# Performance work log

Measured on AMD Instinct MI355X. Metric: run time of the kernel, lower is better.

Reference implementation:

```python
import jax, jax.numpy as jnp
import numpy as np

INPUT_DIM = 4096
BOTTLENECK = 32768
A = 2
K = 0.05
# eval-mode sparsity count: max(1, int(bottleneck * a * k))
K_COUNT = max(1, int(BOTTLENECK * A * K))  # 3276


def setup_inputs() -> dict:
    key = jax.random.key(0)
    kx, kw = jax.random.split(key)
    x = jax.random.normal(kx, (4096, INPUT_DIM), dtype=jnp.float32)
    # encoder weight [bottleneck, input_dim], like nn.Linear(input_dim, bottleneck)
    W = jax.random.normal(kw, (BOTTLENECK, INPUT_DIM), dtype=jnp.float32) * (1.0 / np.sqrt(INPUT_DIM))
    b_enc = jnp.zeros((BOTTLENECK,), dtype=jnp.float32)
    b_dec = jnp.zeros((INPUT_DIM,), dtype=jnp.float32)
    return {"x": x, "W": W, "b_enc": b_enc, "b_dec": b_dec, "epoch": 0}


def reference(x, W, b_enc, b_dec, epoch):
    # encode: z1 = x @ W^T + b_enc  -> [B, bottleneck]
    z1 = jnp.einsum("bi,hi->bh", x, W) + b_enc
    # eval-mode k-winner-take-all mask over dim 1
    _, topk_idx = jax.lax.top_k(z1, K_COUNT)  # [B, K_COUNT]
    rows = jnp.arange(z1.shape[0])[:, None]
    mask = jnp.zeros_like(z1).at[rows, topk_idx].set(1.0)
    a1 = z1 * mask
    # tied-weight decode: z2 = a1 @ W + b_dec -> [B, input_dim]
    z2 = jnp.einsum("bh,hi->bi", a1, W) + b_dec
    return z2
```

## Files before the change

kernel.cpp:

```cpp
#include <hip/hip_runtime.h>
#include <hip/hip_bf16.h>
#include <stdint.h>


#define DIM      4096
#define BATCH    4096
#define NROWS_W  32768
#define KCNT     3276
#define DELTA    0.0025f
#define ROWCAP   256
#define HCAP     64
#define CANDCAP  3584

typedef _Float16 f16x8 __attribute__((ext_vector_type(8)));
typedef _Float16 f16x4 __attribute__((ext_vector_type(4)));
typedef float    f32x4 __attribute__((ext_vector_type(4)));

__device__ __forceinline__ void gload_lds16(const void* g, void* l) {
  __builtin_amdgcn_global_load_lds(
      (const __attribute__((address_space(1))) void*)g,
      (__attribute__((address_space(3))) void*)l, 16, 0, 0);
}

__global__ void k_cvtx(const float* __restrict__ s, _Float16* __restrict__ hi, int n4) {
  int i = blockIdx.x * 256 + threadIdx.x;
  const int stride = gridDim.x * 256;
  for (; i < n4; i += stride) {
    f32x4 v = ((const f32x4*)s)[i];
    f16x4 h;
#pragma unroll
    for (int j = 0; j < 4; ++j) h[j] = (_Float16)v[j];
    ((f16x4*)hi)[i] = h;
  }
}

__global__ void k_splitw(const float* __restrict__ W, _Float16* __restrict__ Wh,
                         _Float16* __restrict__ Wt, f32x4* __restrict__ bcntv) {
  __shared__ _Float16 t[64][65];
  const int c0 = blockIdx.x * 64, r0 = blockIdx.y * 64;
  const int tx = threadIdx.x, ty = threadIdx.y;
  if (blockIdx.y == 0) {
    const int idx = blockIdx.x * 512 + ty * 64 + tx;
    if (idx < 8192) {
      f32x4 z = {0.f, 0.f, 0.f, 0.f};
      bcntv[idx] = z;
    }
  }
  for (int rr = ty; rr < 64; rr += 8) {
    const float w = W[(long)(r0 + rr) * DIM + c0 + tx];
    const _Float16 h = (_Float16)w;
    Wh[(long)(r0 + rr) * DIM + c0 + tx] = h;
    t[rr][tx] = h;
  }
  __syncthreads();
  for (int cc = ty; cc < 64; cc += 8)
    Wt[(long)(c0 + cc) * NROWS_W + r0 + tx] = t[tx][cc];
}

__global__ __launch_bounds__(256, 2)
void k_gemm(const _Float16* __restrict__ A, const _Float16* __restrict__ B,
            const float* __restrict__ bias, float* __restrict__ C,
            int M, int N, int Kt) {
  constexpr int BM = 128, BN = 128, BK = 64;
  __shared__ __align__(16) _Float16 sA[BM * BK];
  __shared__ __align__(16) _Float16 sB[BN * BK];

  const int tid = threadIdx.x;
  const int nbn = N / BN;
  int bm, bn;
  if ((M / BM) % 16 == 0 && nbn % 32 == 0) {
    const int nsbn = nbn / 32;
    const int g = blockIdx.x >> 9, r = blockIdx.x & 511;
    bm = (g / nsbn) * 16 + (r >> 5);
    bn = (g % nsbn) * 32 + (r & 31);
  } else {
    bm = blockIdx.x / nbn;
    bn = blockIdx.x % nbn;
  }
  const int m0 = bm * BM, n0 = bn * BN;
  const int lane = tid & 63, wid = tid >> 6;
  const int wm = wid >> 1, wn = wid & 1;
  const int lr = lane & 15, lk = lane >> 4;
  const int swz = (lr & 7) << 4;

  f32x4 acc[4][4] = {};

  for (int k0 = 0; k0 < Kt; k0 += BK) {
#pragma unroll
    for (int r = 0; r < 4; ++r) {
      const int o = (r * 256 + tid) * 16;
      const int row = o >> 7;
      const int colb = (o & 127) ^ ((row & 7) << 4);
      const long gA = ((long)(m0 + row) * Kt + k0) * 2 + colb;
      const long gB = ((long)(n0 + row) * Kt + k0) * 2 + colb;
      gload_lds16((const char*)A + gA, (char*)sA + o);
      gload_lds16((const char*)B + gB, (char*)sB + o);
    }
    __syncthreads();

#pragma unroll
    for (int kk = 0; kk < 2; ++kk) {
      f16x8 va[4], vb[4];
      const int kbase = (kk * 64 + lk * 16) ^ swz;
#pragma unroll
      for (int m = 0; m < 4; ++m) {
        const int row = wm * 64 + m * 16 + lr;
        va[m] = *(const f16x8*)((const char*)sA + row * 128 + kbase);
      }
#pragma unroll
      for (int n = 0; n < 4; ++n) {
        const int row = wn * 64 + n * 16 + lr;
        vb[n] = *(const f16x8*)((const char*)sB + row * 128 + kbase);
      }
#pragma unroll
      for (int m = 0; m < 4; ++m)
#pragma unroll
        for (int n = 0; n < 4; ++n)
          acc[m][n] = __builtin_amdgcn_mfma_f32_16x16x32_f16(va[m], vb[n], acc[m][n], 0, 0, 0);
    }
    __syncthreads();
  }

#pragma unroll
  for (int n = 0; n < 4; ++n) {
    const int col = n0 + wn * 64 + n * 16 + lr;
    const float bv = bias[col];
#pragma unroll
    for (int m = 0; m < 4; ++m) {
      const int r0r = m0 + wm * 64 + m * 16 + lk * 4;
#pragma unroll
      for (int j = 0; j < 4; ++j)
        C[(long)(r0r + j) * N + col] = acc[m][n][j] + bv;
    }
  }
}

__device__ __forceinline__ unsigned f2o(float f) {
  unsigned b = __float_as_uint(f);
  return ((int)b < 0) ? ~b : (b | 0x80000000u);
}
__device__ __forceinline__ float o2f(unsigned u) {
  unsigned b = (u & 0x80000000u) ? (u & 0x7FFFFFFFu) : ~u;
  return __uint_as_float(b);
}

__global__ __launch_bounds__(256)
void k_topk4(const float* __restrict__ z1, float* __restrict__ thr,
             unsigned* __restrict__ rowlist, unsigned* __restrict__ rowcnt,
             unsigned* __restrict__ c1, unsigned* __restrict__ bucket,
             unsigned* __restrict__ bcnt, _Float16* __restrict__ a1, int kwant) {
  __shared__ unsigned hist[4096];
  __shared__ float cv[CANDCAP];
  __shared__ unsigned short ci[CANDCAP];
  __shared__ unsigned s_n, s_bin, s_rem, s_wt[4], s_cnt, s_above;
  const int tid = threadIdx.x;
  const int b = blockIdx.x;
  const f32x4* zv = (const f32x4*)(z1 + (long)b * NROWS_W);
  constexpr int NV = NROWS_W / 4;

#pragma unroll
  for (int j = 0; j < 16; ++j) hist[tid + j * 256] = 0;
  if (tid == 0) { s_n = 0; s_cnt = 0; s_above = 0; }
  __syncthreads();
  for (int i = tid; i < NV; i += 256) {
    f32x4 v = zv[i];
#pragma unroll
    for (int j = 0; j < 4; ++j) atomicAdd(&hist[f2o(v[j]) >> 20], 1u);
  }
  __syncthreads();
  unsigned p = 0;
#pragma unroll
  for (int j = 0; j < 16; ++j) p += hist[tid * 16 + j];
  unsigned sfx = p;
  const int lane = tid & 63, w = tid >> 6;
#pragma unroll
  for (int off = 1; off < 64; off <<= 1) {
    unsigned o = __shfl_down(sfx, off);
    sfx += (lane + off < 64) ? o : 0u;
  }
  if (lane == 0) s_wt[w] = sfx;
  __syncthreads();
  unsigned above_waves = 0;
  for (int ww = w + 1; ww < 4; ++ww) above_waves += s_wt[ww];
  const unsigned incl = sfx + above_waves;
  const int cnt = __syncthreads_count(incl >= (unsigned)kwant);
  const int tstar = cnt - 1;
  if (tid == tstar) {
    unsigned cum = incl - p;
    int bsel = tid * 16;
    for (int j = 15; j >= 0; --j) {
      const unsigned h = hist[tid * 16 + j];
      if (cum + h >= (unsigned)kwant) { bsel = tid * 16 + j; break; }
      cum += h;
    }
    s_bin = (unsigned)bsel;
    s_rem = (unsigned)kwant - cum;
  }
  __syncthreads();
  const unsigned binsel = s_bin;
  unsigned rem = s_rem;

  const unsigned blo = (binsel > 0) ? binsel - 1 : 0;
  const unsigned bhi = (binsel < 4095) ? binsel + 1 : 4095;
  for (int i = tid; i < NV; i += 256) {
    f32x4 v = zv[i];
#pragma unroll
    for (int j = 0; j < 4; ++j) {
      const unsigned bin = f2o(v[j]) >> 20;
      if (bin >= blo && bin <= bhi) {
        const unsigned jj = atomicAdd(&s_n, 1u);
        if (jj < CANDCAP) { cv[jj] = v[j]; ci[jj] = (unsigned short)(i * 4 + j); }
      }
    }
  }
  __syncthreads();
  const int n = (s_n < CANDCAP) ? (int)s_n : CANDCAP;

  unsigned pfx = 0;
#pragma unroll
  for (int pass = 0; pass < 3; ++pass) {
    const int shift = (pass == 0) ? 12 : (pass == 1) ? 4 : 0;
    const int nb = (pass == 2) ? 16 : 256;
    if (tid < 256) hist[tid] = 0;
    __syncthreads();
    for (int i = tid; i < n; i += 256) {
      const unsigned u = f2o(cv[i]);
      if ((u >> 20) != binsel) continue;
      const unsigned v = u & 0xFFFFFu;
      const bool m = (pass == 0) ? true
                     : (pass == 1) ? ((v >> 12) == (pfx >> 12))
                                   : ((v >> 4) == (pfx >> 4));
      if (m) atomicAdd(&hist[(v >> shift) & (nb - 1)], 1u);
    }
    __syncthreads();
    if (tid == 0) {
      unsigned cum = 0;
      int d = nb - 1;
      for (; d > 0; --d) {
        if (cum + hist[d] >= rem) break;
        cum += hist[d];
      }
      s_bin = (unsigned)d;
      s_rem = rem - cum;
    }
    __syncthreads();
    pfx |= (s_bin << shift);
    rem = s_rem;
    __syncthreads();
  }
  const float t = o2f((binsel << 20) | pfx);
  if (tid == 0) thr[b] = t;
  const float hi = t + DELTA, lo = t - DELTA;

  for (int i = tid; i < n; i += 256) {
    const float v = cv[i];
    if (v >= lo && v <= hi) {
      const unsigned idx = ci[i];
      const unsigned jj = atomicAdd(&s_cnt, 1u);
      if (jj < ROWCAP) {
        rowlist[(long)b * ROWCAP + jj] = idx;
        const unsigned pq = atomicAdd(&bcnt[idx], 1u);
        if (pq < HCAP) bucket[(long)idx * HCAP + pq] = ((unsigned)b << 9) | jj;
      }
    }
  }

  unsigned my_above = 0;
  f16x4* av = (f16x4*)(a1 + (long)b * NROWS_W);
  for (int i = tid; i < NV; i += 256) {
    f32x4 v = zv[i];
    f16x4 o;
#pragma unroll
    for (int j = 0; j < 4; ++j) {
      const bool in = v[j] > hi;
      my_above += in ? 1u : 0u;
      o[j] = in ? (_Float16)v[j] : (_Float16)0.0f;
    }
    av[i] = o;
  }
  atomicAdd(&s_above, my_above);
  __syncthreads();
  if (tid == 0) {
    rowcnt[b] = (s_cnt < ROWCAP) ? s_cnt : ROWCAP;
    c1[b] = s_above;
  }
}

__global__ void k_recompute(const float* __restrict__ W, const float* __restrict__ x,
                            const unsigned* __restrict__ bucket,
                            const unsigned* __restrict__ bcnt,
                            float* __restrict__ exact) {
  const int h = blockIdx.x;
  unsigned n = bcnt[h];
  if (n > HCAP) n = HCAP;
  if (n == 0) return;
  __shared__ float wrec[DIM];
  const long wb = (long)h * DIM;
  for (int i = threadIdx.x; i < DIM / 4; i += 256)
    ((f32x4*)wrec)[i] = ((const f32x4*)(W + wb))[i];
  __syncthreads();
  const int w = threadIdx.x >> 6, lane = threadIdx.x & 63;
  for (unsigned e = w; e < n; e += 4) {
    const unsigned ent = bucket[(long)h * HCAP + e];
    const int b = ent >> 9, j = ent & 511;
    const f32x4* xv = (const f32x4*)(x + (long)b * DIM);
    float s = 0.f;
#pragma unroll
    for (int c = 0; c < 16; ++c) {
      const int i4 = c * 64 + lane;
      f32x4 v = xv[i4];
      const float* wr = &wrec[i4 * 4];
#pragma unroll
      for (int q = 0; q < 4; ++q) s += v[q] * wr[q];
    }
#pragma unroll
    for (int m = 32; m; m >>= 1) s += __shfl_xor(s, m);
    if (lane == 0) exact[(long)b * ROWCAP + j] = s;
  }
}

__global__ void k_select(const float* __restrict__ exact, const unsigned* __restrict__ rowlist,
                         const unsigned* __restrict__ rowcnt, const unsigned* __restrict__ c1,
                         const float* __restrict__ z1, _Float16* __restrict__ a1) {
  const int b = blockIdx.x;
  const int n = (int)rowcnt[b];
  const int need = KCNT - (int)c1[b];
  __shared__ float vals[ROWCAP];
  const int j = threadIdx.x;
  vals[j] = (j < n) ? exact[(long)b * ROWCAP + j] : -1e30f;
  __syncthreads();
  if (j < n) {
    const float vj = vals[j];
    int rank = 0;
    for (int i = 0; i < n; ++i) {
      const float vi = vals[i];
      rank += (vi > vj || (vi == vj && i < j)) ? 1 : 0;
    }
    if (rank < need) {
      const unsigned h = rowlist[(long)b * ROWCAP + j];
      const long off = (long)b * NROWS_W + h;
      a1[off] = (_Float16)z1[off];
    }
  }
}

extern "C" void kernel_launch(void* const* d_in, const int* in_sizes, int n_in,
                              void* d_out, int out_size, void* d_ws, size_t ws_size,
                              hipStream_t stream) {
  const float* x     = (const float*)d_in[0];
  const float* W     = (const float*)d_in[1];
  const float* b_enc = (const float*)d_in[2];
  const float* b_dec = (const float*)d_in[3];
  float* out = (float*)d_out;

  const long NW = (long)NROWS_W * DIM;
  const long NX = (long)BATCH * DIM;
  const long NZ = (long)BATCH * NROWS_W;

  char* ws = (char*)d_ws;
  _Float16* Wh = (_Float16*)ws;
  _Float16* Wt = Wh + NW;
  _Float16* xh = Wt + NW;
  float*  z1 = (float*)(xh + NX);
  float*  thr = z1 + NZ;
  char*   sc = (char*)(thr + BATCH);
  unsigned* rowcnt  = (unsigned*)sc;
  unsigned* c1      = (unsigned*)(sc + 16384);
  unsigned* bcnt    = (unsigned*)(sc + 32768);
  float*    exact   = (float*)(sc + 163840);
  unsigned* rowlist = (unsigned*)(sc + 4358144);
  unsigned* bucket  = (unsigned*)(sc + 8552448);
  _Float16* a1 = Wh;

  const size_t needed = (size_t)(4 * NW + 2 * NX) + (size_t)4 * NZ + 4 * BATCH + 17000000;
  if (ws_size < needed) return;

  k_splitw<<<dim3(DIM / 64, NROWS_W / 64), dim3(64, 8), 0, stream>>>(W, Wh, Wt, (f32x4*)bcnt);
  k_cvtx<<<2048, 256, 0, stream>>>(x, xh, (int)(NX / 4));

  k_gemm<<<(BATCH / 128) * (NROWS_W / 128), 256, 0, stream>>>(
      xh, Wh, b_enc, z1, BATCH, NROWS_W, DIM);

  k_topk4<<<BATCH, 256, 0, stream>>>(z1, thr, rowlist, rowcnt, c1, bucket, bcnt, a1, KCNT);
  k_recompute<<<NROWS_W, 256, 0, stream>>>(W, x, bucket, bcnt, exact);
  k_select<<<BATCH, ROWCAP, 0, stream>>>(exact, rowlist, rowcnt, c1, z1, a1);

  k_gemm<<<(BATCH / 128) * (DIM / 128), 256, 0, stream>>>(
      a1, Wt, b_dec, out, BATCH, DIM, NROWS_W);
}
```

Before: 3.154 ms.

## Fuse a1 writeback into candidate pass, template GEMM with XCD-aware tile remap

Removes the third full pass over each z1 row in top-k. The a1 f16 row is now written during the candidate-collection pass, using bin counts rather than the threshold to decide what is clearly above. Candidates near the boundary are spilled to global memory so k_select can later count and write those above the threshold. The GEMM is templated on its shapes with compile-time dimensions, and block IDs are remapped so consecutive tiles land on the same XCD, with a tunable supertile shape for L2 reuse. This adds a large candidate workspace and extra global traffic in k_select.

```diff
diff --git a/kernel.cpp b/kernel.cpp
--- a/kernel.cpp
+++ b/kernel.cpp
@@ -57,26 +57,26 @@
     Wt[(long)(c0 + cc) * NROWS_W + r0 + tx] = t[tx][cc];
 }
 
+template <int MT, int NTOT, int KT, int SML, int SNL>
 __global__ __launch_bounds__(256, 2)
 void k_gemm(const _Float16* __restrict__ A, const _Float16* __restrict__ B,
-            const float* __restrict__ bias, float* __restrict__ C,
-            int M, int N, int Kt) {
+            const float* __restrict__ bias, float* __restrict__ C) {
   constexpr int BM = 128, BN = 128, BK = 64;
   __shared__ __align__(16) _Float16 sA[BM * BK];
   __shared__ __align__(16) _Float16 sB[BN * BK];
 
   const int tid = threadIdx.x;
-  const int nbn = N / BN;
-  int bm, bn;
-  if ((M / BM) % 16 == 0 && nbn % 32 == 0) {
-    const int nsbn = nbn / 32;
-    const int g = blockIdx.x >> 9, r = blockIdx.x & 511;
-    bm = (g / nsbn) * 16 + (r >> 5);
-    bn = (g % nsbn) * 32 + (r & 31);
-  } else {
-    bm = blockIdx.x / nbn;
-    bn = blockIdx.x % nbn;
-  }
+  constexpr int nbm = MT / BM, nbn = NTOT / BN;
+  constexpr int grid = nbm * nbn;
+  constexpr int nstn = nbn >> SNL;
+  constexpr int stsz = 1 << (SML + SNL);
+
+  int wg = blockIdx.x;
+  wg = (wg & 7) * (grid >> 3) + (wg >> 3);
+  const int g = wg >> (SML + SNL), r = wg & (stsz - 1);
+  const int bm = ((g / nstn) << SML) + (r >> SNL);
+  const int bn = ((g % nstn) << SNL) + (r & ((1 << SNL) - 1));
+
   const int m0 = bm * BM, n0 = bn * BN;
   const int lane = tid & 63, wid = tid >> 6;
   const int wm = wid >> 1, wn = wid & 1;
@@ -85,14 +85,14 @@
 
   f32x4 acc[4][4] = {};
 
-  for (int k0 = 0; k0 < Kt; k0 += BK) {
-#pragma unroll
-    for (int r = 0; r < 4; ++r) {
-      const int o = (r * 256 + tid) * 16;
+  for (int k0 = 0; k0 < KT; k0 += BK) {
+#pragma unroll
+    for (int rr = 0; rr < 4; ++rr) {
+      const int o = (rr * 256 + tid) * 16;
       const int row = o >> 7;
       const int colb = (o & 127) ^ ((row & 7) << 4);
-      const long gA = ((long)(m0 + row) * Kt + k0) * 2 + colb;
-      const long gB = ((long)(n0 + row) * Kt + k0) * 2 + colb;
+      const long gA = ((long)(m0 + row) * KT + k0) * 2 + colb;
+      const long gB = ((long)(n0 + row) * KT + k0) * 2 + colb;
       gload_lds16((const char*)A + gA, (char*)sA + o);
       gload_lds16((const char*)B + gB, (char*)sB + o);
     }
@@ -130,7 +130,7 @@
       const int r0r = m0 + wm * 64 + m * 16 + lk * 4;
 #pragma unroll
       for (int j = 0; j < 4; ++j)
-        C[(long)(r0r + j) * N + col] = acc[m][n][j] + bv;
+        C[(long)(r0r + j) * NTOT + col] = acc[m][n][j] + bv;
     }
   }
 }
@@ -148,7 +148,9 @@
 void k_topk4(const float* __restrict__ z1, float* __restrict__ thr,
              unsigned* __restrict__ rowlist, unsigned* __restrict__ rowcnt,
              unsigned* __restrict__ c1, unsigned* __restrict__ bucket,
-             unsigned* __restrict__ bcnt, _Float16* __restrict__ a1, int kwant) {
+             unsigned* __restrict__ bcnt, _Float16* __restrict__ a1,
+             float* __restrict__ candv, unsigned short* __restrict__ candi,
+             unsigned* __restrict__ candn, int kwant) {
   __shared__ unsigned hist[4096];
   __shared__ float cv[CANDCAP];
   __shared__ unsigned short ci[CANDCAP];
@@ -200,21 +202,40 @@
   const unsigned binsel = s_bin;
   unsigned rem = s_rem;
 
+  {
+    unsigned loc = 0;
+#pragma unroll
+    for (int j = 0; j < 16; ++j) {
+      const unsigned bin = tid * 16 + j;
+      if (bin >= binsel + 2) loc += hist[bin];
+    }
+    if (loc) atomicAdd(&s_above, loc);
+  }
+
   const unsigned blo = (binsel > 0) ? binsel - 1 : 0;
   const unsigned bhi = (binsel < 4095) ? binsel + 1 : 4095;
+  f16x4* av = (f16x4*)(a1 + (long)b * NROWS_W);
   for (int i = tid; i < NV; i += 256) {
     f32x4 v = zv[i];
+    f16x4 o;
 #pragma unroll
     for (int j = 0; j < 4; ++j) {
       const unsigned bin = f2o(v[j]) >> 20;
+      o[j] = (bin > bhi) ? (_Float16)v[j] : (_Float16)0.0f;
       if (bin >= blo && bin <= bhi) {
         const unsigned jj = atomicAdd(&s_n, 1u);
         if (jj < CANDCAP) { cv[jj] = v[j]; ci[jj] = (unsigned short)(i * 4 + j); }
       }
     }
+    av[i] = o;
   }
   __syncthreads();
   const int n = (s_n < CANDCAP) ? (int)s_n : CANDCAP;
+  if (tid == 0) candn[b] = (unsigned)n;
+  for (int i = tid; i < n; i += 256) {
+    candv[(long)b * CANDCAP + i] = cv[i];
+    candi[(long)b * CANDCAP + i] = ci[i];
+  }
 
   unsigned pfx = 0;
 #pragma unroll
@@ -264,21 +285,6 @@
       }
     }
   }
-
-  unsigned my_above = 0;
-  f16x4* av = (f16x4*)(a1 + (long)b * NROWS_W);
-  for (int i = tid; i < NV; i += 256) {
-    f32x4 v = zv[i];
-    f16x4 o;
-#pragma unroll
-    for (int j = 0; j < 4; ++j) {
-      const bool in = v[j] > hi;
-      my_above += in ? 1u : 0u;
-      o[j] = in ? (_Float16)v[j] : (_Float16)0.0f;
-    }
-    av[i] = o;
-  }
-  atomicAdd(&s_above, my_above);
   __syncthreads();
   if (tid == 0) {
     rowcnt[b] = (s_cnt < ROWCAP) ? s_cnt : ROWCAP;
@@ -321,14 +327,26 @@
 
 __global__ void k_select(const float* __restrict__ exact, const unsigned* __restrict__ rowlist,
                          const unsigned* __restrict__ rowcnt, const unsigned* __restrict__ c1,
+                         const float* __restrict__ thr, const float* __restrict__ candv,
+                         const unsigned short* __restrict__ candi,
+                         const unsigned* __restrict__ candn,
                          const float* __restrict__ z1, _Float16* __restrict__ a1) {
   const int b = blockIdx.x;
   const int n = (int)rowcnt[b];
-  const int need = KCNT - (int)c1[b];
+  const int nc = (int)candn[b];
+  const float t = thr[b];
+  const float hi = t + DELTA;
   __shared__ float vals[ROWCAP];
+  __shared__ unsigned s_c;
   const int j = threadIdx.x;
+  if (j == 0) s_c = 0;
   vals[j] = (j < n) ? exact[(long)b * ROWCAP + j] : -1e30f;
   __syncthreads();
+  unsigned loc = 0;
+  for (int i = j; i < nc; i += 256) loc += (candv[(long)b * CANDCAP + i] > hi) ? 1u : 0u;
+  if (loc) atomicAdd(&s_c, loc);
+  __syncthreads();
+  const int need = KCNT - (int)c1[b] - (int)s_c;
   if (j < n) {
     const float vj = vals[j];
     int rank = 0;
@@ -341,6 +359,10 @@
       const long off = (long)b * NROWS_W + h;
       a1[off] = (_Float16)z1[off];
     }
+  }
+  for (int i = j; i < nc; i += 256) {
+    const float v = candv[(long)b * CANDCAP + i];
+    if (v > hi) a1[(long)b * NROWS_W + candi[(long)b * CANDCAP + i]] = (_Float16)v;
   }
 }
 
@@ -370,21 +392,26 @@
   float*    exact   = (float*)(sc + 163840);
   unsigned* rowlist = (unsigned*)(sc + 4358144);
   unsigned* bucket  = (unsigned*)(sc + 8552448);
+  unsigned* candn   = (unsigned*)(sc + 16941056);
+  float*    candv   = (float*)(sc + 16957440);
+  unsigned short* candi = (unsigned short*)(sc + 75677696);
   _Float16* a1 = Wh;
 
-  const size_t needed = (size_t)(4 * NW + 2 * NX) + (size_t)4 * NZ + 4 * BATCH + 17000000;
+  const size_t needed = (size_t)(4 * NW + 2 * NX) + (size_t)4 * NZ + 4 * BATCH + 106000000;
   if (ws_size < needed) return;
 
   k_splitw<<<dim3(DIM / 64, NROWS_W / 64), dim3(64, 8), 0, stream>>>(W, Wh, Wt, (f32x4*)bcnt);
   k_cvtx<<<2048, 256, 0, stream>>>(x, xh, (int)(NX / 4));
 
-  k_gemm<<<(BATCH / 128) * (NROWS_W / 128), 256, 0, stream>>>(
-      xh, Wh, b_enc, z1, BATCH, NROWS_W, DIM);
-
-  k_topk4<<<BATCH, 256, 0, stream>>>(z1, thr, rowlist, rowcnt, c1, bucket, bcnt, a1, KCNT);
+  k_gemm<BATCH, NROWS_W, DIM, 4, 5>
+      <<<(BATCH / 128) * (NROWS_W / 128), 256, 0, stream>>>(xh, Wh, b_enc, z1);
+
+  k_topk4<<<BATCH, 256, 0, stream>>>(z1, thr, rowlist, rowcnt, c1, bucket, bcnt,
+                                     a1, candv, candi, candn, KCNT);
   k_recompute<<<NROWS_W, 256, 0, stream>>>(W, x, bucket, bcnt, exact);
-  k_select<<<BATCH, ROWCAP, 0, stream>>>(exact, rowlist, rowcnt, c1, z1, a1);
-
-  k_gemm<<<(BATCH / 128) * (DIM / 128), 256, 0, stream>>>(
-      a1, Wt, b_dec, out, BATCH, DIM, NROWS_W);
-}
+  k_select<<<BATCH, ROWCAP, 0, stream>>>(exact, rowlist, rowcnt, c1, thr,
+                                         candv, candi, candn, z1, a1);
+
+  k_gemm<BATCH, DIM, NROWS_W, 4, 3>
+      <<<(BATCH / 128) * (DIM / 128), 256, 0, stream>>>(a1, Wt, b_dec, out);
+}
```

Result: slower. 3.433 ms (+8.8%).
